# Kernel tuning notes

Measured on AMD Instinct MI355X. Metric: run time of the kernel, lower is better.

Reference implementation:

```python
import jax, jax.numpy as jnp
import numpy as np

B, C, H, W = 64, 256, 56, 56
SCALES = (1, 2, 4, 8)  # scale[:groups] with groups=4; sum = 15 pooled maps


def setup_inputs() -> dict:
    key = jax.random.key(0)
    k1, k2 = jax.random.split(key)
    x = jax.random.normal(k1, (B, C, H, W), dtype=jnp.float32)
    # weight: [num_fea=H*W, sum(scales)=15]; small init (original fills 0, which
    # would make the gate identically sigmoid(0)=0.5 — use small random instead)
    weight = jax.random.normal(k2, (H * W, 15), dtype=jnp.float32) * 0.02
    return {"x": x, "weight": weight}


def reference(x, weight):
    b, c, h, w = x.shape
    hw = h * w
    # Multi-scale channel-group mean pooling: for scale i, split channels into
    # i equal groups (c divisible by all scales) and mean over each group.
    # Equivalent to the original's loop of c*j//i : c*(j+1)//i slices.
    feats = [x.reshape(b, i, c // i, hw).mean(axis=2) for i in SCALES]
    t = jnp.concatenate(feats, axis=1)  # [b, 15, hw]
    # Points(): normalize across the 15 pooled features per spatial location
    mean = t.mean(axis=1, keepdims=True)           # [b, 1, hw]
    std = t.std(axis=1, keepdims=True)             # unbiased=False (ddof=0)
    tn = (t - mean) / std                          # [b, 15, hw]
    # _style_integration: per-pixel weighted sum over the 15 features
    z = jnp.einsum('bfs,sf->bs', tn, weight)       # [b, hw]
    gate = jax.nn.sigmoid(z).reshape(b, 1, h, w)
    return x * gate
```

## Files before the change

kernel.cpp:

```cpp
#include <hip/hip_runtime.h>
#include <math.h>


constexpr int C_   = 256;
constexpr int HW_  = 3136;
constexpr int B_   = 64;
constexpr int SPW_ = 16;
constexpr int TPI_ = HW_ / SPW_;
constexpr int WPB_ = 16;

__device__ __forceinline__ float4 shx4(float4 a, int m) {
  float4 r;
  r.x = __shfl_xor(a.x, m);
  r.y = __shfl_xor(a.y, m);
  r.z = __shfl_xor(a.z, m);
  r.w = __shfl_xor(a.w, m);
  return r;
}
__device__ __forceinline__ float4 add4(float4 a, float4 b) {
  float4 r; r.x = a.x + b.x; r.y = a.y + b.y; r.z = a.z + b.z; r.w = a.w + b.w;
  return r;
}

__global__ __launch_bounds__(1024, 4) void ppca_fused(
    const float* __restrict__ x, const float* __restrict__ wgt,
    float* __restrict__ out)
{
  const int lane = threadIdx.x & 63;
  const int wav  = threadIdx.x >> 6;
  const unsigned W   = blockIdx.x * WPB_ + wav;
  const unsigned b   = W / TPI_;
  const unsigned til = W - b * TPI_;
  const int sp0 = til * SPW_;

  const int s4 = lane & 3;
  const int c0 = lane >> 2;

  const size_t off = (size_t)b * C_ * HW_ + (size_t)c0 * 16 * HW_
                   + (size_t)sp0 + (size_t)(s4 << 2);
  const float* xb = x + off;
  float* ob = out + off;

  float4 v[16];
  #pragma unroll
  for (int i = 0; i < 16; ++i)
    v[i] = *(const float4*)(xb + (size_t)i * HW_);

  float4 ps = v[0];
  #pragma unroll
  for (int i = 1; i < 16; ++i) ps = add4(ps, v[i]);

  const float4 t1 = add4(ps, shx4(ps, 4));
  const float4 t2 = add4(t1, shx4(t1, 8));
  const float4 t3 = add4(t2, shx4(t2, 16));
  const float4 t4 = add4(t3, shx4(t3, 32));

  float4 m4;
  m4.x = t4.x * (1.f / 256.f); m4.y = t4.y * (1.f / 256.f);
  m4.z = t4.z * (1.f / 256.f); m4.w = t4.w * (1.f / 256.f);

  const float* wr = wgt + (size_t)sp0 * 15;
  const int i128 = 1 + (c0 >> 3);
  const int i64  = 3 + (c0 >> 2);
  const int i32  = 7 + (c0 >> 1);

  float4 zn, sq;
#define DO_SPATIAL(J, T1c, T2c, T3c, Mc, ZNc, SQc)                           \
  {                                                                          \
    const float* wp = wr + ((s4 << 2) + J) * 15;                             \
    const float w128 = wp[i128];                                             \
    const float w64  = wp[i64];                                              \
    const float w32  = wp[i32];                                              \
    const float u1 = T1c * (1.f / 32.f)  - Mc;                               \
    const float u2 = T2c * (1.f / 64.f)  - Mc;                               \
    const float u3 = T3c * (1.f / 128.f) - Mc;                               \
    ZNc = u1 * w32 * 0.5f + u2 * w64 * 0.25f + u3 * w128 * 0.125f;           \
    SQc = u1 * u1 * 0.5f + u2 * u2 * 0.25f + u3 * u3 * 0.125f;               \
  }
  DO_SPATIAL(0, t1.x, t2.x, t3.x, m4.x, zn.x, sq.x)
  DO_SPATIAL(1, t1.y, t2.y, t3.y, m4.y, zn.y, sq.y)
  DO_SPATIAL(2, t1.z, t2.z, t3.z, m4.z, zn.z, sq.z)
  DO_SPATIAL(3, t1.w, t2.w, t3.w, m4.w, zn.w, sq.w)
#undef DO_SPATIAL

  #pragma unroll
  for (int d = 4; d <= 32; d <<= 1) {
    zn = add4(zn, shx4(zn, d));
    sq = add4(sq, shx4(sq, d));
  }

  float4 g;
#define GATE(ZNc, SQc, Gc)                                                   \
  {                                                                          \
    const float inv = 1.f / sqrtf(SQc * (1.f / 15.f));                       \
    Gc = 1.f / (1.f + __expf(-(ZNc * inv)));                                 \
  }
  GATE(zn.x, sq.x, g.x)
  GATE(zn.y, sq.y, g.y)
  GATE(zn.z, sq.z, g.z)
  GATE(zn.w, sq.w, g.w)
#undef GATE

  #pragma unroll
  for (int i = 0; i < 16; ++i) {
    float4 vv = v[i];
    vv.x *= g.x; vv.y *= g.y; vv.z *= g.z; vv.w *= g.w;
    *(float4*)(ob + (size_t)i * HW_) = vv;
  }
}

extern "C" void kernel_launch(void* const* d_in, const int* in_sizes, int n_in,
                              void* d_out, int out_size, void* d_ws, size_t ws_size,
                              hipStream_t stream) {
  const float* x = (const float*)d_in[0];
  const float* w = (const float*)d_in[1];
  float* out = (float*)d_out;
  (void)in_sizes; (void)n_in; (void)out_size; (void)d_ws; (void)ws_size;

  dim3 grid(B_ * TPI_ / WPB_);
  dim3 block(1024);
  ppca_fused<<<grid, block, 0, stream>>>(x, w, out);
}
```

Baseline: 357.9 us.

## Split channels across four waves per 64-pixel tile with LDS group reduction

Each 256-thread block now covers 64 contiguous spatial positions, with each wave handling 64 channels. Lanes are arranged so 16 lanes span 64 floats of one channel row, where before 4 lanes spanned 16 floats. Cross-wave group sums are combined through shared memory with one barrier, replacing the all-lane shuffle tree. The aim is wider contiguous memory segments per row and fewer shuffles. The cost is a block-wide sync, LDS traffic and smaller blocks.

```diff
diff --git a/kernel.cpp b/kernel.cpp
--- a/kernel.cpp
+++ b/kernel.cpp
@@ -5,9 +5,8 @@
 constexpr int C_   = 256;
 constexpr int HW_  = 3136;
 constexpr int B_   = 64;
-constexpr int SPW_ = 16;
-constexpr int TPI_ = HW_ / SPW_;
-constexpr int WPB_ = 16;
+constexpr int SPB_ = 64;
+constexpr int TPI_ = HW_ / SPB_;
 
 __device__ __forceinline__ float4 shx4(float4 a, int m) {
   float4 r;
@@ -22,24 +21,27 @@
   return r;
 }
 
-__global__ __launch_bounds__(1024, 4) void ppca_fused(
+__global__ __launch_bounds__(256, 4) void ppca_fused(
     const float* __restrict__ x, const float* __restrict__ wgt,
     float* __restrict__ out)
 {
+  __shared__ __align__(16) float S[8 * SPB_];
+
   const int lane = threadIdx.x & 63;
   const int wav  = threadIdx.x >> 6;
-  const unsigned W   = blockIdx.x * WPB_ + wav;
-  const unsigned b   = W / TPI_;
-  const unsigned til = W - b * TPI_;
-  const int sp0 = til * SPW_;
+  const unsigned blk = blockIdx.x;
+  const unsigned b   = blk / TPI_;
+  const unsigned til = blk - b * TPI_;
+  const int sp0 = til * SPB_;
 
-  const int s4 = lane & 3;
-  const int c0 = lane >> 2;
+  const int s4 = lane & 15;
+  const int c0 = lane >> 4;
 
-  const size_t off = (size_t)b * C_ * HW_ + (size_t)c0 * 16 * HW_
-                   + (size_t)sp0 + (size_t)(s4 << 2);
-  const float* xb = x + off;
-  float* ob = out + off;
+  const int chbase = wav * 64 + c0 * 16;
+  const size_t base = (size_t)b * C_ * HW_ + (size_t)chbase * HW_
+                    + (size_t)sp0 + (size_t)(s4 << 2);
+  const float* xb = x + base;
+  float* ob = out + base;
 
   float4 v[16];
   #pragma unroll
@@ -50,44 +52,87 @@
   #pragma unroll
   for (int i = 1; i < 16; ++i) ps = add4(ps, v[i]);
 
-  const float4 t1 = add4(ps, shx4(ps, 4));
-  const float4 t2 = add4(t1, shx4(t1, 8));
-  const float4 t3 = add4(t2, shx4(t2, 16));
-  const float4 t4 = add4(t3, shx4(t3, 32));
+  const float4 t32 = add4(ps, shx4(ps, 16));
+
+  if ((c0 & 1) == 0) {
+    const int g = 2 * wav + (c0 >> 1);
+    *(float4*)(&S[g * SPB_ + (s4 << 2)]) = t32;
+  }
+  __syncthreads();
+
+  float4 T = {0.f, 0.f, 0.f, 0.f};
+  float4 H;
+  #pragma unroll
+  for (int g = 0; g < 8; ++g) {
+    const float4 q = *(const float4*)(&S[g * SPB_ + (s4 << 2)]);
+    T = add4(T, q);
+    if (g == 3) H = T;
+  }
+  const float4 gA = *(const float4*)(&S[(2 * c0)     * SPB_ + (s4 << 2)]);
+  const float4 gB = *(const float4*)(&S[(2 * c0 + 1) * SPB_ + (s4 << 2)]);
 
   float4 m4;
-  m4.x = t4.x * (1.f / 256.f); m4.y = t4.y * (1.f / 256.f);
-  m4.z = t4.z * (1.f / 256.f); m4.w = t4.w * (1.f / 256.f);
+  m4.x = T.x * (1.f / 256.f); m4.y = T.y * (1.f / 256.f);
+  m4.z = T.z * (1.f / 256.f); m4.w = T.w * (1.f / 256.f);
 
-  const float* wr = wgt + (size_t)sp0 * 15;
-  const int i128 = 1 + (c0 >> 3);
-  const int i64  = 3 + (c0 >> 2);
-  const int i32  = 7 + (c0 >> 1);
+  float4 uA, uB, u64, u128;
+#define CF(Fc, Sc, SCALE, Mc) Fc = Sc * (1.f / SCALE) - Mc;
+  CF(uA.x, gA.x, 32.f, m4.x) CF(uA.y, gA.y, 32.f, m4.y)
+  CF(uA.z, gA.z, 32.f, m4.z) CF(uA.w, gA.w, 32.f, m4.w)
+  CF(uB.x, gB.x, 32.f, m4.x) CF(uB.y, gB.y, 32.f, m4.y)
+  CF(uB.z, gB.z, 32.f, m4.z) CF(uB.w, gB.w, 32.f, m4.w)
+#undef CF
+  {
+    const float4 g64 = add4(gA, gB);
+    u64.x = g64.x * (1.f / 64.f) - m4.x;
+    u64.y = g64.y * (1.f / 64.f) - m4.y;
+    u64.z = g64.z * (1.f / 64.f) - m4.z;
+    u64.w = g64.w * (1.f / 64.f) - m4.w;
+  }
+  if (c0 == 1) {
+    u128.x = H.x * (1.f / 128.f) - m4.x;
+    u128.y = H.y * (1.f / 128.f) - m4.y;
+    u128.z = H.z * (1.f / 128.f) - m4.z;
+    u128.w = H.w * (1.f / 128.f) - m4.w;
+  } else if (c0 == 3) {
+    u128.x = (T.x - H.x) * (1.f / 128.f) - m4.x;
+    u128.y = (T.y - H.y) * (1.f / 128.f) - m4.y;
+    u128.z = (T.z - H.z) * (1.f / 128.f) - m4.z;
+    u128.w = (T.w - H.w) * (1.f / 128.f) - m4.w;
+  } else {
+    u128.x = 0.f; u128.y = 0.f; u128.z = 0.f; u128.w = 0.f;
+  }
 
-  float4 zn, sq;
-#define DO_SPATIAL(J, T1c, T2c, T3c, Mc, ZNc, SQc)                           \
+  float4 sq;
+#define SQC(Qc, Ac, Bc, Cc, Dc) Qc = Ac*Ac + Bc*Bc + Cc*Cc + Dc*Dc;
+  SQC(sq.x, uA.x, uB.x, u64.x, u128.x)
+  SQC(sq.y, uA.y, uB.y, u64.y, u128.y)
+  SQC(sq.z, uA.z, uB.z, u64.z, u128.z)
+  SQC(sq.w, uA.w, uB.w, u64.w, u128.w)
+#undef SQC
+
+  const int iA   = 7 + 2 * c0;
+  const int iB   = 8 + 2 * c0;
+  const int i64  = 3 + c0;
+  const int i128 = 1 + (c0 >> 1);
+  const float* wr = wgt + (size_t)(sp0 + (s4 << 2)) * 15;
+
+  float4 zn;
+#define ZNC(J, Zc, Ac, Bc, Cc, Dc)                                           \
   {                                                                          \
-    const float* wp = wr + ((s4 << 2) + J) * 15;                             \
-    const float w128 = wp[i128];                                             \
-    const float w64  = wp[i64];                                              \
-    const float w32  = wp[i32];                                              \
-    const float u1 = T1c * (1.f / 32.f)  - Mc;                               \
-    const float u2 = T2c * (1.f / 64.f)  - Mc;                               \
-    const float u3 = T3c * (1.f / 128.f) - Mc;                               \
-    ZNc = u1 * w32 * 0.5f + u2 * w64 * 0.25f + u3 * w128 * 0.125f;           \
-    SQc = u1 * u1 * 0.5f + u2 * u2 * 0.25f + u3 * u3 * 0.125f;               \
+    const float* wp = wr + (J) * 15;                                         \
+    Zc = Ac * wp[iA] + Bc * wp[iB] + Cc * wp[i64] + Dc * wp[i128];           \
   }
-  DO_SPATIAL(0, t1.x, t2.x, t3.x, m4.x, zn.x, sq.x)
-  DO_SPATIAL(1, t1.y, t2.y, t3.y, m4.y, zn.y, sq.y)
-  DO_SPATIAL(2, t1.z, t2.z, t3.z, m4.z, zn.z, sq.z)
-  DO_SPATIAL(3, t1.w, t2.w, t3.w, m4.w, zn.w, sq.w)
-#undef DO_SPATIAL
+  ZNC(0, zn.x, uA.x, uB.x, u64.x, u128.x)
+  ZNC(1, zn.y, uA.y, uB.y, u64.y, u128.y)
+  ZNC(2, zn.z, uA.z, uB.z, u64.z, u128.z)
+  ZNC(3, zn.w, uA.w, uB.w, u64.w, u128.w)
+#undef ZNC
 
-  #pragma unroll
-  for (int d = 4; d <= 32; d <<= 1) {
-    zn = add4(zn, shx4(zn, d));
-    sq = add4(sq, shx4(sq, d));
-  }
+  zn = add4(zn, shx4(zn, 16));
+  sq = add4(sq, shx4(sq, 16));
+  zn = add4(zn, shx4(zn, 32));
+  sq = add4(sq, shx4(sq, 32));
 
   float4 g;
 #define GATE(ZNc, SQc, Gc)                                                   \
@@ -117,7 +162,7 @@
   float* out = (float*)d_out;
   (void)in_sizes; (void)n_in; (void)out_size; (void)d_ws; (void)ws_size;
 
-  dim3 grid(B_ * TPI_ / WPB_);
-  dim3 block(1024);
+  dim3 grid(B_ * TPI_);
+  dim3 block(256);
   ppca_fused<<<grid, block, 0, stream>>>(x, w, out);
 }
```

New measurement: 340.8 us. 4.8% less time.
